# Optimization experiments

Measured on AMD Instinct MI355X. Metric: run time of the kernel, lower is better.

The kernel has to match this reference:

```python
import jax, jax.numpy as jnp
import numpy as np

E = 256
H_HEADS = 8
HD = E // H_HEADS
NEG = -1e9


def setup_inputs() -> dict:
    key = jax.random.key(0)
    ks = jax.random.split(key, 16)
    B, Q, Hh, Ww = 16, 100, 64, 64
    S = Hh * Ww
    std = 1.0 / np.sqrt(E)
    inp = {
        "query_features": jax.random.normal(ks[0], (B, Q, E), jnp.float32),
        "image_features": jax.random.normal(ks[1], (B, E, Hh, Ww), jnp.float32),
        "mask": jax.random.randint(ks[2], (B, Q, Hh, Ww), 0, 2) > 0,
        "pos_query_embeddings": jax.random.normal(ks[3], (B, Q, E), jnp.float32),
        "pos_image_embeddings": jax.random.normal(ks[4], (B, S, E), jnp.float32),
        "Wq": jax.random.normal(ks[5], (E, E), jnp.float32) * std,
        "bq": jnp.zeros((E,), jnp.float32),
        "Wk": jax.random.normal(ks[6], (E, E), jnp.float32) * std,
        "bk": jnp.zeros((E,), jnp.float32),
        "Wv": jax.random.normal(ks[7], (E, E), jnp.float32) * std,
        "bv": jnp.zeros((E,), jnp.float32),
        "Wo": jax.random.normal(ks[8], (E, E), jnp.float32) * std,
        "bo": jnp.zeros((E,), jnp.float32),
    }
    return inp


def reference(query_features, image_features, mask, pos_query_embeddings,
              pos_image_embeddings, Wq, bq, Wk, bk, Wv, bv, Wo, bo):
    B, _, Hh, Ww = image_features.shape
    Q = query_features.shape[1]
    S = Hh * Ww
    # (B, S, E)
    img = jnp.transpose(image_features.reshape(B, E, S), (0, 2, 1))
    q = (query_features + pos_query_embeddings) @ Wq.T + bq  # (B,Q,E)
    k = (img + pos_image_embeddings) @ Wk.T + bk              # (B,S,E)
    v = img @ Wv.T + bv                                       # (B,S,E)
    q = q.reshape(B, Q, H_HEADS, HD).transpose(0, 2, 1, 3)    # (B,H,Q,D)
    k = k.reshape(B, S, H_HEADS, HD).transpose(0, 2, 1, 3)    # (B,H,S,D)
    v = v.reshape(B, S, H_HEADS, HD).transpose(0, 2, 1, 3)
    scale = 1.0 / jnp.sqrt(jnp.asarray(HD, q.dtype))
    scores = jnp.einsum('bhqd,bhsd->bhqs', q, k) * scale
    amask = mask.reshape(B, 1, Q, S)
    scores = jnp.where(amask, scores, NEG)
    attn = jax.nn.softmax(scores, axis=-1)
    out = jnp.einsum('bhqs,bhsd->bhqd', attn, v)
    out = out.transpose(0, 2, 1, 3).reshape(B, Q, E)
    return out @ Wo.T + bo
```

## Files before the change

### kernel.cpp

```cpp
#include <hip/hip_runtime.h>
#include <math.h>

#define BB 16
#define QQ 100
#define EE 256
#define NH 8
#define HD 32
#define SS 4096
#define QP 128
#define NZ 8
#define SCHUNK (SS / NZ)
#define M0 8.0f

typedef _Float16 half8_t __attribute__((ext_vector_type(8)));
typedef _Float16 half4_t __attribute__((ext_vector_type(4)));
typedef float floatx4 __attribute__((ext_vector_type(4)));

__global__ __launch_bounds__(256) void maskpack_kernel(
    const int* __restrict__ mask, unsigned* __restrict__ mbits)
{
    int gid  = blockIdx.x * 256 + threadIdx.x;
    int lane = gid & 63;
    int F    = gid & ~63;
    int s    = (F & (SS - 1)) + lane;
    int qp   = (F >> 12) & (QP - 1);
    int b    = F >> 19;
    int qc   = min(qp, QQ - 1);
    int v    = mask[((size_t)(b * QQ + qc)) * SS + s];
    unsigned long long bal = __ballot(v != 0);
    int w = (F & (SS - 1)) >> 5;
    if (lane == 0)
        mbits[((size_t)(b * (SS / 32) + w)) * QP + qp] = (unsigned)bal;
    if (lane == 32)
        mbits[((size_t)(b * (SS / 32) + w + 1)) * QP + qp] = (unsigned)(bal >> 32);
}

__global__ __launch_bounds__(256, 2) void fused_kv_kernel(
    const float* __restrict__ img,
    const float* __restrict__ pos,
    const float* __restrict__ Wk, const float* __restrict__ bk,
    const float* __restrict__ Wv, const float* __restrict__ bv,
    _Float16* __restrict__ kbuf,
    _Float16* __restrict__ vt)
{
    __shared__ _Float16 smem[2 * 64 * 40 + 2 * 256 * 40];
    _Float16* Ak = smem;
    _Float16* Av = Ak + 64 * 40;
    _Float16* Bk = Av + 64 * 40;
    _Float16* Bv = Bk + 256 * 40;

    const int t  = threadIdx.x;
    const int w  = t >> 6;
    const int l  = t & 63;
    const int gg = l >> 4, li = l & 15;

    const int m0 = blockIdx.x * 64;
    const int b  = m0 >> 12;
    const int s0 = m0 & (SS - 1);

    const float* imgb = img + (size_t)b * EE * SS + s0;
    const float* posb = pos + ((size_t)b * SS + s0) * EE;

    const int sf8 = t & 3;
    const int ss  = t >> 2;

    floatx4 acck[4][4] = {};
    floatx4 accv[4][4] = {};

    float iv[8], pv[8];
    {
        const float* ic = imgb + (size_t)(sf8 * 8) * SS + ss;
        #pragma unroll
        for (int j = 0; j < 8; ++j) iv[j] = ic[(size_t)j * SS];
        float4 p0 = *(const float4*)(posb + (size_t)ss * EE + sf8 * 8);
        float4 p1 = *(const float4*)(posb + (size_t)ss * EE + sf8 * 8 + 4);
        pv[0]=p0.x; pv[1]=p0.y; pv[2]=p0.z; pv[3]=p0.w;
        pv[4]=p1.x; pv[5]=p1.y; pv[6]=p1.z; pv[7]=p1.w;
    }

    #pragma unroll 1
    for (int kk = 0; kk < 8; ++kk) {
        const int f0 = kk * 32;
        {
            half8_t hv, hk;
            #pragma unroll
            for (int j = 0; j < 8; ++j) {
                hv[j] = (_Float16)iv[j];
                hk[j] = (_Float16)(iv[j] + pv[j]);
            }
            *(half8_t*)&Av[ss * 40 + sf8 * 8] = hv;
            *(half8_t*)&Ak[ss * 40 + sf8 * 8] = hk;
        }
        #pragma unroll
        for (int c = 0; c < 8; ++c) {
            int r = (c & 3) * 64 + (t >> 2);
            const float* src = ((c < 4) ? Wk : Wv) + (size_t)r * EE + f0 + sf8 * 8;
            float4 a0 = *(const float4*)src;
            float4 a1 = *(const float4*)(src + 4);
            half8_t hw;
            hw[0]=(_Float16)a0.x; hw[1]=(_Float16)a0.y;
            hw[2]=(_Float16)a0.z; hw[3]=(_Float16)a0.w;
            hw[4]=(_Float16)a1.x; hw[5]=(_Float16)a1.y;
            hw[6]=(_Float16)a1.z; hw[7]=(_Float16)a1.w;
            _Float16* dst = (c < 4) ? Bk : Bv;
            *(half8_t*)&dst[r * 40 + sf8 * 8] = hw;
        }
        __syncthreads();

        if (kk < 7) {
            const int f1 = f0 + 32;
            const float* ic = imgb + (size_t)(f1 + sf8 * 8) * SS + ss;
            #pragma unroll
            for (int j = 0; j < 8; ++j) iv[j] = ic[(size_t)j * SS];
            float4 p0 = *(const float4*)(posb + (size_t)ss * EE + f1 + sf8 * 8);
            float4 p1 = *(const float4*)(posb + (size_t)ss * EE + f1 + sf8 * 8 + 4);
            pv[0]=p0.x; pv[1]=p0.y; pv[2]=p0.z; pv[3]=p0.w;
            pv[4]=p1.x; pv[5]=p1.y; pv[6]=p1.z; pv[7]=p1.w;
        }

        {
            half8_t af[4], bf[4];
            #pragma unroll
            for (int i = 0; i < 4; ++i) {
                af[i] = *(const half8_t*)&Ak[(i * 16 + li) * 40 + gg * 8];
                bf[i] = *(const half8_t*)&Bk[(w * 64 + i * 16 + li) * 40 + gg * 8];
            }
            #pragma unroll
            for (int i = 0; i < 4; ++i)
                #pragma unroll
                for (int j = 0; j < 4; ++j)
                    acck[i][j] = __builtin_amdgcn_mfma_f32_16x16x32_f16(
                        af[i], bf[j], acck[i][j], 0, 0, 0);
        }
        {
            half8_t af[4], bf[4];
            #pragma unroll
            for (int i = 0; i < 4; ++i) {
                af[i] = *(const half8_t*)&Av[(i * 16 + li) * 40 + gg * 8];
                bf[i] = *(const half8_t*)&Bv[(w * 64 + i * 16 + li) * 40 + gg * 8];
            }
            #pragma unroll
            for (int i = 0; i < 4; ++i)
                #pragma unroll
                for (int j = 0; j < 4; ++j)
                    accv[i][j] = __builtin_amdgcn_mfma_f32_16x16x32_f16(
                        af[i], bf[j], accv[i][j], 0, 0, 0);
        }
        __syncthreads();
    }

    #pragma unroll
    for (int j = 0; j < 4; ++j) {
        int e = w * 64 + j * 16 + li;
        float bj = bk[e];
        #pragma unroll
        for (int i = 0; i < 4; ++i) {
            int row = m0 + i * 16 + gg * 4;
            #pragma unroll
            for (int r = 0; r < 4; ++r)
                kbuf[(size_t)(row + r) * EE + e] = (_Float16)(acck[i][j][r] + bj);
        }
    }

    _Float16* vstage = smem;
    #pragma unroll
    for (int j = 0; j < 4; ++j) {
        int e_loc = w * 64 + j * 16 + li;
        float bj = bv[e_loc];
        #pragma unroll
        for (int i = 0; i < 4; ++i) {
            int s_loc = i * 16 + gg * 4;
            half4_t h4;
            #pragma unroll
            for (int r = 0; r < 4; ++r)
                h4[r] = (_Float16)(accv[i][j][r] + bj);
            *(half4_t*)&vstage[e_loc * 72 + s_loc] = h4;
        }
    }
    __syncthreads();
    #pragma unroll
    for (int c = 0; c < 8; ++c) {
        int row = c * 32 + (t >> 3);
        int so  = (t & 7) * 8;
        half8_t v8 = *(const half8_t*)&vstage[row * 72 + so];
        int hh = row >> 5, dd = row & 31;
        *(half8_t*)(vt + ((size_t)((b * NH + hh) * HD + dd)) * SS + s0 + so) = v8;
    }
}

__global__ __launch_bounds__(256) void proj_kernel(
    const float* __restrict__ x1, const float* __restrict__ x2,
    const float* __restrict__ W, const float* __restrict__ bias,
    float* __restrict__ outf, _Float16* __restrict__ out16,
    float oscale, int has_x2)
{
    const int row0 = blockIdx.x * 8;
    const int t = threadIdx.x;
    __shared__ float xs[8][256];

    #pragma unroll
    for (int p = 0; p < 8; ++p) {
        int idx = t + p * 256;
        int f = idx & 255, j = idx >> 8;
        size_t g = (size_t)(row0 + j) * EE + f;
        float v = x1[g];
        if (has_x2) v += x2[g];
        xs[j][f] = v;
    }
    __syncthreads();

    const int e = t;
    const float* wrow = W + (size_t)e * EE;
    float acc[8];
    const float bv = bias[e];
    #pragma unroll
    for (int j = 0; j < 8; ++j) acc[j] = bv;

    #pragma unroll 4
    for (int f4 = 0; f4 < 64; ++f4) {
        float4 w4 = *(const float4*)(wrow + f4 * 4);
        #pragma unroll
        for (int j = 0; j < 8; ++j) {
            float4 x4 = *(const float4*)&xs[j][f4 * 4];
            acc[j] = fmaf(w4.x, x4.x, acc[j]);
            acc[j] = fmaf(w4.y, x4.y, acc[j]);
            acc[j] = fmaf(w4.z, x4.z, acc[j]);
            acc[j] = fmaf(w4.w, x4.w, acc[j]);
        }
    }
    if (out16) {
        #pragma unroll
        for (int j = 0; j < 8; ++j)
            out16[(size_t)(row0 + j) * EE + e] = (_Float16)(acc[j] * oscale);
    } else {
        #pragma unroll
        for (int j = 0; j < 8; ++j)
            outf[(size_t)(row0 + j) * EE + e] = acc[j];
    }
}

__global__ __launch_bounds__(256) void attn_mfma_kernel(
    const _Float16* __restrict__ q16,
    const _Float16* __restrict__ kbuf,
    const _Float16* __restrict__ vt,
    const unsigned* __restrict__ mbits,
    float* __restrict__ part,
    float* __restrict__ pl)
{
    const int z = blockIdx.x, h = blockIdx.y, b = blockIdx.z;
    const int t = threadIdx.x;
    const int w = t >> 6, l = t & 63;
    const int g = l >> 4, li = l & 15;

    __shared__ _Float16 ks[64 * 40];
    __shared__ _Float16 vs[32 * 72];
    __shared__ _Float16 ps[128 * 72];
    __shared__ unsigned mw[2][QP];

    half8_t qf[2];
    {
        int q0r = min(32 * w + li, QQ - 1);
        int q1r = min(32 * w + 16 + li, QQ - 1);
        qf[0] = *(const half8_t*)(q16 + ((size_t)(b * QQ + q0r)) * EE + h * HD + g * 8);
        qf[1] = *(const half8_t*)(q16 + ((size_t)(b * QQ + q1r)) * EE + h * HD + g * 8);
    }

    float lsum[2][4] = {{0.f}};
    floatx4 accO[2][2] = {};

    for (int it = 0; it < SCHUNK / 64; ++it) {
        const int sblk = z * SCHUNK + it * 64;

        {
            int sl = t >> 2, koff = (t & 3) * 8;
            *(half8_t*)&ks[sl * 40 + koff] =
                *(const half8_t*)(kbuf + ((size_t)(b * SS + sblk + sl)) * EE + h * HD + koff);
            int dl = t >> 3, soff = (t & 7) * 8;
            *(half8_t*)&vs[dl * 72 + soff] =
                *(const half8_t*)(vt + ((size_t)((b * NH + h) * HD + dl)) * SS + sblk + soff);
            mw[t >> 7][t & 127] =
                mbits[((size_t)(b * (SS / 32) + (sblk >> 5) + (t >> 7))) * QP + (t & 127)];
        }
        __syncthreads();

        half8_t kf[4];
        #pragma unroll
        for (int st = 0; st < 4; ++st)
            kf[st] = *(const half8_t*)&ks[(st * 16 + li) * 40 + g * 8];
        floatx4 sc[2][4];
        #pragma unroll
        for (int qt = 0; qt < 2; ++qt)
            #pragma unroll
            for (int st = 0; st < 4; ++st) {
                floatx4 zero = {0.f, 0.f, 0.f, 0.f};
                sc[qt][st] = __builtin_amdgcn_mfma_f32_16x16x32_f16(
                    qf[qt], kf[st], zero, 0, 0, 0);
            }

        #pragma unroll
        for (int qt = 0; qt < 2; ++qt) {
            int qrow0 = 32 * w + qt * 16 + 4 * g;
            unsigned w0r[4], w1r[4];
            #pragma unroll
            for (int r = 0; r < 4; ++r) {
                w0r[r] = mw[0][qrow0 + r];
                w1r[r] = mw[1][qrow0 + r];
            }
            #pragma unroll
            for (int st = 0; st < 4; ++st)
                #pragma unroll
                for (int r = 0; r < 4; ++r) {
                    unsigned word = (st < 2) ? w0r[r] : w1r[r];
                    int keep = (word >> ((st & 1) * 16 + li)) & 1;
                    float pv = keep ? __expf(sc[qt][st][r] - M0) : 0.f;
                    _Float16 ph = (_Float16)pv;
                    lsum[qt][r] += (float)ph;
                    ps[(qrow0 + r) * 72 + st * 16 + li] = ph;
                }
        }

        half8_t vb[2][2];
        #pragma unroll
        for (int dt = 0; dt < 2; ++dt) {
            vb[dt][0] = *(const half8_t*)&vs[(dt * 16 + li) * 72 + g * 8];
            vb[dt][1] = *(const half8_t*)&vs[(dt * 16 + li) * 72 + 32 + g * 8];
        }
        #pragma unroll
        for (int qt = 0; qt < 2; ++qt) {
            half8_t a0 = *(const half8_t*)&ps[(32 * w + qt * 16 + li) * 72 + g * 8];
            half8_t a1 = *(const half8_t*)&ps[(32 * w + qt * 16 + li) * 72 + 32 + g * 8];
            #pragma unroll
            for (int dt = 0; dt < 2; ++dt) {
                accO[qt][dt] = __builtin_amdgcn_mfma_f32_16x16x32_f16(
                    a0, vb[dt][0], accO[qt][dt], 0, 0, 0);
                accO[qt][dt] = __builtin_amdgcn_mfma_f32_16x16x32_f16(
                    a1, vb[dt][1], accO[qt][dt], 0, 0, 0);
            }
        }
        __syncthreads();
    }

    #pragma unroll
    for (int qt = 0; qt < 2; ++qt)
        #pragma unroll
        for (int r = 0; r < 4; ++r) {
            float v = lsum[qt][r];
            v += __shfl_xor(v, 1, 64);
            v += __shfl_xor(v, 2, 64);
            v += __shfl_xor(v, 4, 64);
            v += __shfl_xor(v, 8, 64);
            lsum[qt][r] = v;
        }

    const size_t pbase = (((size_t)z * BB + b) * NH + h) * QP;
    #pragma unroll
    for (int qt = 0; qt < 2; ++qt) {
        int qrow0 = 32 * w + qt * 16 + 4 * g;
        #pragma unroll
        for (int r = 0; r < 4; ++r) {
            int qp = qrow0 + r;
            #pragma unroll
            for (int dt = 0; dt < 2; ++dt)
                part[(pbase + qp) * HD + dt * 16 + li] = accO[qt][dt][r];
            if (li == 0) pl[pbase + qp] = lsum[qt][r];
        }
    }
}

__global__ __launch_bounds__(256) void combine_kernel(
    const float* __restrict__ part, const float* __restrict__ pl,
    float* __restrict__ abuf)
{
    int tid = blockIdx.x * 256 + threadIdx.x;
    int d  = tid & 31;
    int qp = (tid >> 5) & 127;
    int h  = (tid >> 12) & 7;
    int b  = tid >> 15;
    if (qp >= QQ) return;
    float L = 0.f, O = 0.f;
    #pragma unroll
    for (int zz = 0; zz < NZ; ++zz) {
        size_t idx = (((size_t)zz * BB + b) * NH + h) * QP + qp;
        L += pl[idx];
        O += part[idx * HD + d];
    }
    abuf[((size_t)(b * QQ + qp)) * EE + h * HD + d] = O / fmaxf(L, 1e-30f);
}

extern "C" void kernel_launch(void* const* d_in, const int* in_sizes, int n_in,
                              void* d_out, int out_size, void* d_ws, size_t ws_size,
                              hipStream_t stream)
{
    const float* qf   = (const float*)d_in[0];
    const float* img  = (const float*)d_in[1];
    const int*   mask = (const int*)  d_in[2];
    const float* pq   = (const float*)d_in[3];
    const float* pimg = (const float*)d_in[4];
    const float* Wq   = (const float*)d_in[5];
    const float* bq   = (const float*)d_in[6];
    const float* Wk   = (const float*)d_in[7];
    const float* bk   = (const float*)d_in[8];
    const float* Wv   = (const float*)d_in[9];
    const float* bv   = (const float*)d_in[10];
    const float* Wo   = (const float*)d_in[11];
    const float* bo   = (const float*)d_in[12];
    float* out = (float*)d_out;

    const size_t MSE = (size_t)BB * SS * EE;

    _Float16* kbuf = (_Float16*)d_ws;
    _Float16* vtb  = kbuf + MSE;
    _Float16* q16  = vtb + MSE;
    unsigned* mbits = (unsigned*)(q16 + (size_t)BB * QQ * EE);
    float* part = (float*)(mbits + (size_t)BB * (SS / 32) * QP);
    float* pl   = part + (size_t)NZ * BB * NH * QP * HD;
    float* abuf = pl + (size_t)NZ * BB * NH * QP;

    const float scale = 0.17677669529663687f;

    maskpack_kernel<<<(BB * QP * SS) / 256, 256, 0, stream>>>(mask, mbits);
    proj_kernel<<<BB * QQ / 8, 256, 0, stream>>>(qf, pq, Wq, bq, nullptr, q16, scale, 1);
    fused_kv_kernel<<<BB * SS / 64, 256, 0, stream>>>(img, pimg, Wk, bk, Wv, bv, kbuf, vtb);
    attn_mfma_kernel<<<dim3(NZ, NH, BB), 256, 0, stream>>>(q16, kbuf, vtb, mbits, part, pl);
    combine_kernel<<<(BB * NH * QP * HD) / 256, 256, 0, stream>>>(part, pl, abuf);
    proj_kernel<<<BB * QQ / 8, 256, 0, stream>>>(abuf, nullptr, Wo, bo, out, nullptr, 1.f, 0);
}
```

Before: 310.9 us.

## Restructure KV projection: 512 threads, register weight fragments, double-buffered A tile

The fused K/V projection kernel moves to 512 threads with 8 waves, and each wave now covers 32 output features instead of 64. Weight fragments are loaded straight from global memory into registers and converted to fp16, no longer staged through shared memory. The activation tile is double-buffered in shared memory, so each k-step needs only one barrier instead of two. This shrinks shared memory and accumulator registers to allow more resident blocks, at the cost of redundant global weight reads across blocks and waves, which should stay cache-resident.

```diff
diff --git a/kernel.cpp b/kernel.cpp
--- a/kernel.cpp
+++ b/kernel.cpp
@@ -35,7 +35,7 @@
         mbits[((size_t)(b * (SS / 32) + w + 1)) * QP + qp] = (unsigned)(bal >> 32);
 }
 
-__global__ __launch_bounds__(256, 2) void fused_kv_kernel(
+__global__ __launch_bounds__(512, 3) void fused_kv_kernel(
     const float* __restrict__ img,
     const float* __restrict__ pos,
     const float* __restrict__ Wk, const float* __restrict__ bk,
@@ -43,11 +43,7 @@
     _Float16* __restrict__ kbuf,
     _Float16* __restrict__ vt)
 {
-    __shared__ _Float16 smem[2 * 64 * 40 + 2 * 256 * 40];
-    _Float16* Ak = smem;
-    _Float16* Av = Ak + 64 * 40;
-    _Float16* Bk = Av + 64 * 40;
-    _Float16* Bv = Bk + 256 * 40;
+    __shared__ _Float16 smem[256 * 72];
 
     const int t  = threadIdx.x;
     const int w  = t >> 6;
@@ -58,114 +54,116 @@
     const int b  = m0 >> 12;
     const int s0 = m0 & (SS - 1);
 
-    const float* imgb = img + (size_t)b * EE * SS + s0;
-    const float* posb = pos + ((size_t)b * SS + s0) * EE;
-
-    const int sf8 = t & 3;
-    const int ss  = t >> 2;
-
-    floatx4 acck[4][4] = {};
-    floatx4 accv[4][4] = {};
-
-    float iv[8], pv[8];
+    const float* imgb = img + (size_t)b * EE * SS + s0 + l;
+    const float* posb = pos + ((size_t)b * SS + s0 + l) * EE + w * 4;
+
+    floatx4 acck[4][2] = {};
+    floatx4 accv[4][2] = {};
+
+    float iv[4], pv[4];
     {
-        const float* ic = imgb + (size_t)(sf8 * 8) * SS + ss;
-        #pragma unroll
-        for (int j = 0; j < 8; ++j) iv[j] = ic[(size_t)j * SS];
-        float4 p0 = *(const float4*)(posb + (size_t)ss * EE + sf8 * 8);
-        float4 p1 = *(const float4*)(posb + (size_t)ss * EE + sf8 * 8 + 4);
-        pv[0]=p0.x; pv[1]=p0.y; pv[2]=p0.z; pv[3]=p0.w;
-        pv[4]=p1.x; pv[5]=p1.y; pv[6]=p1.z; pv[7]=p1.w;
+        #pragma unroll
+        for (int j = 0; j < 4; ++j) iv[j] = imgb[(size_t)(w * 4 + j) * SS];
+        float4 p = *(const float4*)posb;
+        pv[0] = p.x; pv[1] = p.y; pv[2] = p.z; pv[3] = p.w;
     }
 
     #pragma unroll 1
     for (int kk = 0; kk < 8; ++kk) {
+        _Float16* Ak = smem + (kk & 1) * 5120;
+        _Float16* Av = Ak + 2560;
         const int f0 = kk * 32;
+
         {
-            half8_t hv, hk;
-            #pragma unroll
-            for (int j = 0; j < 8; ++j) {
+            half4_t hk, hv;
+            #pragma unroll
+            for (int j = 0; j < 4; ++j) {
                 hv[j] = (_Float16)iv[j];
                 hk[j] = (_Float16)(iv[j] + pv[j]);
             }
-            *(half8_t*)&Av[ss * 40 + sf8 * 8] = hv;
-            *(half8_t*)&Ak[ss * 40 + sf8 * 8] = hk;
-        }
-        #pragma unroll
-        for (int c = 0; c < 8; ++c) {
-            int r = (c & 3) * 64 + (t >> 2);
-            const float* src = ((c < 4) ? Wk : Wv) + (size_t)r * EE + f0 + sf8 * 8;
-            float4 a0 = *(const float4*)src;
-            float4 a1 = *(const float4*)(src + 4);
-            half8_t hw;
-            hw[0]=(_Float16)a0.x; hw[1]=(_Float16)a0.y;
-            hw[2]=(_Float16)a0.z; hw[3]=(_Float16)a0.w;
-            hw[4]=(_Float16)a1.x; hw[5]=(_Float16)a1.y;
-            hw[6]=(_Float16)a1.z; hw[7]=(_Float16)a1.w;
-            _Float16* dst = (c < 4) ? Bk : Bv;
-            *(half8_t*)&dst[r * 40 + sf8 * 8] = hw;
+            *(half4_t*)&Av[l * 40 + w * 4] = hv;
+            *(half4_t*)&Ak[l * 40 + w * 4] = hk;
         }
         __syncthreads();
 
         if (kk < 7) {
             const int f1 = f0 + 32;
-            const float* ic = imgb + (size_t)(f1 + sf8 * 8) * SS + ss;
-            #pragma unroll
-            for (int j = 0; j < 8; ++j) iv[j] = ic[(size_t)j * SS];
-            float4 p0 = *(const float4*)(posb + (size_t)ss * EE + f1 + sf8 * 8);
-            float4 p1 = *(const float4*)(posb + (size_t)ss * EE + f1 + sf8 * 8 + 4);
-            pv[0]=p0.x; pv[1]=p0.y; pv[2]=p0.z; pv[3]=p0.w;
-            pv[4]=p1.x; pv[5]=p1.y; pv[6]=p1.z; pv[7]=p1.w;
+            #pragma unroll
+            for (int j = 0; j < 4; ++j) iv[j] = imgb[(size_t)(f1 + w * 4 + j) * SS];
+            float4 p = *(const float4*)(posb + f1);
+            pv[0] = p.x; pv[1] = p.y; pv[2] = p.z; pv[3] = p.w;
         }
 
         {
-            half8_t af[4], bf[4];
-            #pragma unroll
-            for (int i = 0; i < 4; ++i) {
+            half8_t bf[2];
+            #pragma unroll
+            for (int jj = 0; jj < 2; ++jj) {
+                const float* src = Wk + (size_t)(w * 32 + jj * 16 + li) * EE + f0 + gg * 8;
+                float4 a0 = *(const float4*)src;
+                float4 a1 = *(const float4*)(src + 4);
+                half8_t hw;
+                hw[0]=(_Float16)a0.x; hw[1]=(_Float16)a0.y;
+                hw[2]=(_Float16)a0.z; hw[3]=(_Float16)a0.w;
+                hw[4]=(_Float16)a1.x; hw[5]=(_Float16)a1.y;
+                hw[6]=(_Float16)a1.z; hw[7]=(_Float16)a1.w;
+                bf[jj] = hw;
+            }
+            half8_t af[4];
+            #pragma unroll
+            for (int i = 0; i < 4; ++i)
                 af[i] = *(const half8_t*)&Ak[(i * 16 + li) * 40 + gg * 8];
-                bf[i] = *(const half8_t*)&Bk[(w * 64 + i * 16 + li) * 40 + gg * 8];
-            }
             #pragma unroll
             for (int i = 0; i < 4; ++i)
                 #pragma unroll
-                for (int j = 0; j < 4; ++j)
-                    acck[i][j] = __builtin_amdgcn_mfma_f32_16x16x32_f16(
-                        af[i], bf[j], acck[i][j], 0, 0, 0);
+                for (int jj = 0; jj < 2; ++jj)
+                    acck[i][jj] = __builtin_amdgcn_mfma_f32_16x16x32_f16(
+                        af[i], bf[jj], acck[i][jj], 0, 0, 0);
         }
         {
-            half8_t af[4], bf[4];
-            #pragma unroll
-            for (int i = 0; i < 4; ++i) {
+            half8_t bf[2];
+            #pragma unroll
+            for (int jj = 0; jj < 2; ++jj) {
+                const float* src = Wv + (size_t)(w * 32 + jj * 16 + li) * EE + f0 + gg * 8;
+                float4 a0 = *(const float4*)src;
+                float4 a1 = *(const float4*)(src + 4);
+                half8_t hw;
+                hw[0]=(_Float16)a0.x; hw[1]=(_Float16)a0.y;
+                hw[2]=(_Float16)a0.z; hw[3]=(_Float16)a0.w;
+                hw[4]=(_Float16)a1.x; hw[5]=(_Float16)a1.y;
+                hw[6]=(_Float16)a1.z; hw[7]=(_Float16)a1.w;
+                bf[jj] = hw;
+            }
+            half8_t af[4];
+            #pragma unroll
+            for (int i = 0; i < 4; ++i)
                 af[i] = *(const half8_t*)&Av[(i * 16 + li) * 40 + gg * 8];
-                bf[i] = *(const half8_t*)&Bv[(w * 64 + i * 16 + li) * 40 + gg * 8];
-            }
             #pragma unroll
             for (int i = 0; i < 4; ++i)
                 #pragma unroll
-                for (int j = 0; j < 4; ++j)
-                    accv[i][j] = __builtin_amdgcn_mfma_f32_16x16x32_f16(
-                        af[i], bf[j], accv[i][j], 0, 0, 0);
-        }
-        __syncthreads();
-    }
-
-    #pragma unroll
-    for (int j = 0; j < 4; ++j) {
-        int e = w * 64 + j * 16 + li;
+                for (int jj = 0; jj < 2; ++jj)
+                    accv[i][jj] = __builtin_amdgcn_mfma_f32_16x16x32_f16(
+                        af[i], bf[jj], accv[i][jj], 0, 0, 0);
+        }
+    }
+
+    #pragma unroll
+    for (int jj = 0; jj < 2; ++jj) {
+        int e = w * 32 + jj * 16 + li;
         float bj = bk[e];
         #pragma unroll
         for (int i = 0; i < 4; ++i) {
             int row = m0 + i * 16 + gg * 4;
             #pragma unroll
             for (int r = 0; r < 4; ++r)
-                kbuf[(size_t)(row + r) * EE + e] = (_Float16)(acck[i][j][r] + bj);
-        }
-    }
-
+                kbuf[(size_t)(row + r) * EE + e] = (_Float16)(acck[i][jj][r] + bj);
+        }
+    }
+
+    __syncthreads();
     _Float16* vstage = smem;
     #pragma unroll
-    for (int j = 0; j < 4; ++j) {
-        int e_loc = w * 64 + j * 16 + li;
+    for (int jj = 0; jj < 2; ++jj) {
+        int e_loc = w * 32 + jj * 16 + li;
         float bj = bv[e_loc];
         #pragma unroll
         for (int i = 0; i < 4; ++i) {
@@ -173,14 +171,14 @@
             half4_t h4;
             #pragma unroll
             for (int r = 0; r < 4; ++r)
-                h4[r] = (_Float16)(accv[i][j][r] + bj);
+                h4[r] = (_Float16)(accv[i][jj][r] + bj);
             *(half4_t*)&vstage[e_loc * 72 + s_loc] = h4;
         }
     }
     __syncthreads();
     #pragma unroll
-    for (int c = 0; c < 8; ++c) {
-        int row = c * 32 + (t >> 3);
+    for (int c = 0; c < 4; ++c) {
+        int row = c * 64 + (t >> 3);
         int so  = (t & 7) * 8;
         half8_t v8 = *(const half8_t*)&vstage[row * 72 + so];
         int hh = row >> 5, dd = row & 31;
@@ -420,7 +418,7 @@
 
     maskpack_kernel<<<(BB * QP * SS) / 256, 256, 0, stream>>>(mask, mbits);
     proj_kernel<<<BB * QQ / 8, 256, 0, stream>>>(qf, pq, Wq, bq, nullptr, q16, scale, 1);
-    fused_kv_kernel<<<BB * SS / 64, 256, 0, stream>>>(img, pimg, Wk, bk, Wv, bv, kbuf, vtb);
+    fused_kv_kernel<<<BB * SS / 64, 512, 0, stream>>>(img, pimg, Wk, bk, Wv, bv, kbuf, vtb);
     attn_mfma_kernel<<<dim3(NZ, NH, BB), 256, 0, stream>>>(q16, kbuf, vtb, mbits, part, pl);
     combine_kernel<<<(BB * NH * QP * HD) / 256, 256, 0, stream>>>(part, pl, abuf);
     proj_kernel<<<BB * QQ / 8, 256, 0, stream>>>(abuf, nullptr, Wo, bo, out, nullptr, 1.f, 0);
```

Result: slower. 338.7 us (+9.0%).
